# Kernel optimization log

Hardware: AMD Instinct MI355X
Metric: run time of the kernel (lower is better)

Reference implementation:

```python
import jax, jax.numpy as jnp
import numpy as np

B, S, D, H = 2, 2048, 1024, 16
HD = D // H  # head_dim = 64


def setup_inputs() -> dict:
    key = jax.random.key(0)
    ks = jax.random.split(key, 10)
    sc = 1.0 / np.sqrt(D)
    x = jax.random.normal(ks[0], (B, S, D), dtype=jnp.float32)
    # causal mask, 0 = masked (module does masked_fill(mask == 0, -1e9))
    mask = jnp.broadcast_to(jnp.tril(jnp.ones((S, S), dtype=jnp.int32)), (B, S, S))
    return {
        "x": x,
        "mask": mask,
        "Wq": jax.random.normal(ks[1], (D, D), dtype=jnp.float32) * sc,
        "bq": jnp.zeros((D,), dtype=jnp.float32),
        "Wk": jax.random.normal(ks[2], (D, D), dtype=jnp.float32) * sc,
        "bk": jnp.zeros((D,), dtype=jnp.float32),
        "Wv": jax.random.normal(ks[3], (D, D), dtype=jnp.float32) * sc,
        "bv": jnp.zeros((D,), dtype=jnp.float32),
        "Wo": jax.random.normal(ks[4], (D, D), dtype=jnp.float32) * sc,
        "bo": jnp.zeros((D,), dtype=jnp.float32),
    }


def reference(x, mask, Wq, bq, Wk, bk, Wv, bv, Wo, bo):
    b, s, _ = x.shape
    # torch nn.Linear: y = x @ W.T + b
    def split_heads(t):
        return t.reshape(b, s, H, HD).transpose(0, 2, 1, 3)  # [B,H,S,hd]
    q = split_heads(x @ Wq.T + bq)
    k = split_heads(x @ Wk.T + bk)
    v = split_heads(x @ Wv.T + bv)
    scores = jnp.einsum("bhqd,bhkd->bhqk", q, k) / jnp.sqrt(jnp.float32(HD))
    scores = jnp.where(mask[:, None, :, :] == 0, jnp.float32(-1e9), scores)
    w = jax.nn.softmax(scores, axis=-1)
    out = jnp.einsum("bhqk,bhkd->bhqd", w, v)  # [B,H,S,hd]
    out = out.transpose(0, 2, 1, 3).reshape(b, s, D)
    return out @ Wo.T + bo
```

## Files before the change

kernel.cpp:

```cpp
#include <hip/hip_runtime.h>
#include <cstdint>


typedef __bf16 bf16x8 __attribute__((ext_vector_type(8)));
typedef float f32x4 __attribute__((ext_vector_type(4)));

__device__ inline f32x4 mfma16(bf16x8 a, bf16x8 b, f32x4 c) {
    return __builtin_amdgcn_mfma_f32_16x16x32_bf16(a, b, c, 0, 0, 0);
}

__device__ inline uint16_t f2bf(float f) {
    uint32_t u = __builtin_bit_cast(uint32_t, f);
    u += 0x7FFFu + ((u >> 16) & 1u);
    return (uint16_t)(u >> 16);
}

__device__ inline void gload_lds16(const uint16_t* g, uint16_t* l) {
    __builtin_amdgcn_global_load_lds(
        (const __attribute__((address_space(1))) uint32_t*)g,
        (__attribute__((address_space(3))) uint32_t*)l, 16, 0, 0);
}

__global__ __launch_bounds__(256) void cast_all(const float* __restrict__ x,
                                                const float* __restrict__ wq,
                                                const float* __restrict__ wk,
                                                const float* __restrict__ wv,
                                                const float* __restrict__ wo,
                                                uint16_t* __restrict__ xbf,
                                                uint16_t* __restrict__ wbf) {
    int i = blockIdx.x * 256 + threadIdx.x;
    float4 v;
    uint64_t* dp;
    if (i < (1 << 20)) {
        v = ((const float4*)x)[i];
        dp = (uint64_t*)xbf + i;
    } else {
        int j = i - (1 << 20);
        const float* ws[4] = {wq, wk, wv, wo};
        v = ((const float4*)ws[j >> 18])[j & 0x3FFFF];
        dp = (uint64_t*)wbf + j;
    }
    uint64_t p = (uint64_t)f2bf(v.x) | ((uint64_t)f2bf(v.y) << 16) |
                 ((uint64_t)f2bf(v.z) << 32) | ((uint64_t)f2bf(v.w) << 48);
    *dp = p;
}

template<int OUTF32>
__global__ __launch_bounds__(256) void gemm128(const uint16_t* __restrict__ A,
                                               const uint16_t* __restrict__ W,
                                               const float* __restrict__ b0,
                                               const float* __restrict__ b1,
                                               const float* __restrict__ b2,
                                               void* __restrict__ o0,
                                               void* __restrict__ o1,
                                               void* __restrict__ o2,
                                               int K, float s0, float s1, float s2) {
    __shared__ __align__(16) uint16_t Alds[2][128 * 32];
    __shared__ __align__(16) uint16_t Blds[2][128 * 32];
    const int tid = threadIdx.x;
    const int lane = tid & 63, w = tid >> 6;
    const int l16 = lane & 15, quad = lane >> 4;
    const int wm = w & 1, wn = w >> 1;
    const int m0 = blockIdx.x * 128, n0 = blockIdx.y * 128;

    f32x4 acc[4][4] = {};

    const int ci0 = w * 128 + lane;
    const uint16_t* ga0 = A + (size_t)(m0 + (ci0 >> 2)) * K + (ci0 & 3) * 8;
    const uint16_t* gb0 = W + (size_t)(n0 + (ci0 >> 2)) * K + (ci0 & 3) * 8;
    const int ci1 = ci0 + 64;
    const uint16_t* ga1 = A + (size_t)(m0 + (ci1 >> 2)) * K + (ci1 & 3) * 8;
    const uint16_t* gb1 = W + (size_t)(n0 + (ci1 >> 2)) * K + (ci1 & 3) * 8;

    gload_lds16(ga0, Alds[0] + (w * 2 + 0) * 512);
    gload_lds16(gb0, Blds[0] + (w * 2 + 0) * 512);
    gload_lds16(ga1, Alds[0] + (w * 2 + 1) * 512);
    gload_lds16(gb1, Blds[0] + (w * 2 + 1) * 512);

    const int niter = K >> 5;
    for (int i = 0; i < niter; ++i) {
        __syncthreads();
        if (i + 1 < niter) {
            const int k1 = (i + 1) << 5;
            uint16_t* Ad = Alds[(i + 1) & 1];
            uint16_t* Bd = Blds[(i + 1) & 1];
            gload_lds16(ga0 + k1, Ad + (w * 2 + 0) * 512);
            gload_lds16(gb0 + k1, Bd + (w * 2 + 0) * 512);
            gload_lds16(ga1 + k1, Ad + (w * 2 + 1) * 512);
            gload_lds16(gb1 + k1, Bd + (w * 2 + 1) * 512);
        }
        const uint16_t* Ab = Alds[i & 1];
        const uint16_t* Bb = Blds[i & 1];
        bf16x8 af[4], bw[4];
#pragma unroll
        for (int t = 0; t < 4; ++t) {
            af[t] = *(const bf16x8*)(Ab + (wm * 64 + t * 16 + l16) * 32 + quad * 8);
            bw[t] = *(const bf16x8*)(Bb + (wn * 64 + t * 16 + l16) * 32 + quad * 8);
        }
#pragma unroll
        for (int mt = 0; mt < 4; ++mt)
#pragma unroll
            for (int nt = 0; nt < 4; ++nt)
                acc[mt][nt] = mfma16(af[mt], bw[nt], acc[mt][nt]);
    }

#pragma unroll
    for (int nt = 0; nt < 4; ++nt) {
        int col = n0 + wn * 64 + nt * 16 + l16;
        int seg = col >> 10, lcol = col & 1023;
        const float* bp = (seg == 0) ? b0 : (seg == 1 ? b1 : b2);
        float scale    = (seg == 0) ? s0 : (seg == 1 ? s1 : s2);
        void* op       = (seg == 0) ? o0 : (seg == 1 ? o1 : o2);
        float bc = bp[lcol];
#pragma unroll
        for (int mt = 0; mt < 4; ++mt)
#pragma unroll
            for (int r = 0; r < 4; ++r) {
                int row = m0 + wm * 64 + mt * 16 + quad * 4 + r;
                float v = (acc[mt][nt][r] + bc) * scale;
                if (OUTF32) ((float*)op)[(size_t)row * 1024 + lcol] = v;
                else        ((uint16_t*)op)[(size_t)row * 1024 + lcol] = f2bf(v);
            }
    }
}

__global__ __launch_bounds__(256) void transpose_v(const uint16_t* __restrict__ V,
                                                   uint16_t* __restrict__ Vt) {
    __shared__ __align__(16) uint16_t T[64 * 72];
    const int s0 = blockIdx.x * 64;
    const int bh = blockIdx.y;
    const int b = bh >> 4, h = bh & 15;
    const int tid = threadIdx.x;
    const int r = tid >> 2, c = tid & 3;
#pragma unroll
    for (int half = 0; half < 2; ++half) {
        uint4 v = *(const uint4*)(V + (size_t)(b * 2048 + s0 + r) * 1024 + h * 64 + half * 32 + c * 8);
        *(uint4*)(T + r * 72 + half * 32 + c * 8) = v;
    }
    __syncthreads();
#pragma unroll
    for (int it = 0; it < 2; ++it) {
        int id = it * 256 + tid;
        int d = id >> 3, c8 = (id & 7) * 8;
        uint32_t wpk[4];
#pragma unroll
        for (int jj = 0; jj < 4; ++jj) {
            uint32_t lo = T[(c8 + 2 * jj) * 72 + d];
            uint32_t hi = T[(c8 + 2 * jj + 1) * 72 + d];
            wpk[jj] = lo | (hi << 16);
        }
        uint4 o; o.x = wpk[0]; o.y = wpk[1]; o.z = wpk[2]; o.w = wpk[3];
        *(uint4*)(Vt + ((size_t)bh * 64 + d) * 2048 + s0 + c8) = o;
    }
}

__global__ __launch_bounds__(256) void attn_kernel(const uint16_t* __restrict__ Q,
                                                   const uint16_t* __restrict__ K,
                                                   const uint16_t* __restrict__ Vt,
                                                   uint16_t* __restrict__ att) {
    const int S = 2048, D = 1024;
    __shared__ __align__(16) uint16_t Klds[2][64 * 72];
    __shared__ __align__(16) uint16_t Vlds[2][64 * 72];
    __shared__ __align__(16) uint16_t Plds[4 * 32 * 72];

    const int bh = blockIdx.y;
    const int qb = (bh & 16) ? (int)blockIdx.x : 15 - (int)blockIdx.x;
    const int niter = 2 * qb + 2, kb_diag = 2 * qb;

    const int b = bh >> 4, h = bh & 15;
    const int tid = threadIdx.x, lane = tid & 63, w = tid >> 6;
    const int l16 = lane & 15, quad = lane >> 4;
    const int q0 = qb * 128;
    const size_t baseQK = (size_t)b * S * D + h * 64;
    uint16_t* Pw = Plds + w * (32 * 72);

    bf16x8 aq[2][2];
#pragma unroll
    for (int mt = 0; mt < 2; ++mt)
#pragma unroll
        for (int c = 0; c < 2; ++c)
            aq[mt][c] = *(const bf16x8*)(Q + baseQK +
                (size_t)(q0 + w * 32 + mt * 16 + l16) * D + c * 32 + quad * 8);

    bf16x8 ones;
#pragma unroll
    for (int j = 0; j < 8; ++j) ones[j] = (__bf16)1.0f;

    f32x4 accO[2][4] = {};
    f32x4 accL[2] = {};

    const int srow = tid >> 2, scq = tid & 3;
    const uint16_t* Kg = K + baseQK + (size_t)srow * D + scq * 16;
    const uint16_t* Vg = Vt + ((size_t)bh * 64 + srow) * S + scq * 16;
    const int soff = srow * 72 + scq * 16;

    uint4 kA, kB, vA, vB;
    kA = *(const uint4*)Kg; kB = *(const uint4*)(Kg + 8);
    vA = *(const uint4*)Vg; vB = *(const uint4*)(Vg + 8);
    *(uint4*)(Klds[0] + soff)     = kA;
    *(uint4*)(Klds[0] + soff + 8) = kB;
    *(uint4*)(Vlds[0] + soff)     = vA;
    *(uint4*)(Vlds[0] + soff + 8) = vB;
    {
        const uint16_t* kg = Kg + (size_t)64 * D;
        const uint16_t* vg = Vg + 64;
        kA = *(const uint4*)kg; kB = *(const uint4*)(kg + 8);
        vA = *(const uint4*)vg; vB = *(const uint4*)(vg + 8);
    }
    __syncthreads();

    for (int kb = 0; kb < niter; ++kb) {
        const uint16_t* Kb = Klds[kb & 1];
        const uint16_t* Vb = Vlds[kb & 1];

        if (kb + 1 < niter) {
            uint16_t* Kd = (uint16_t*)Klds[(kb + 1) & 1];
            uint16_t* Vd = (uint16_t*)Vlds[(kb + 1) & 1];
            *(uint4*)(Kd + soff)     = kA;
            *(uint4*)(Kd + soff + 8) = kB;
            *(uint4*)(Vd + soff)     = vA;
            *(uint4*)(Vd + soff + 8) = vB;
            if (kb + 2 < niter) {
                const uint16_t* kg = Kg + (size_t)((kb + 2) * 64) * D;
                const uint16_t* vg = Vg + (kb + 2) * 64;
                kA = *(const uint4*)kg; kB = *(const uint4*)(kg + 8);
                vA = *(const uint4*)vg; vB = *(const uint4*)(vg + 8);
            }
        }

        f32x4 sc[2][4];
#pragma unroll
        for (int t = 0; t < 4; ++t) {
            bf16x8 bk0 = *(const bf16x8*)(Kb + (t * 16 + l16) * 72 + quad * 8);
            bf16x8 bk1 = *(const bf16x8*)(Kb + (t * 16 + l16) * 72 + 32 + quad * 8);
            f32x4 z0 = {}; f32x4 z1 = {};
            sc[0][t] = mfma16(aq[0][1], bk1, mfma16(aq[0][0], bk0, z0));
            sc[1][t] = mfma16(aq[1][1], bk1, mfma16(aq[1][0], bk0, z1));
        }

        bf16x8 bv0[4], bv1[4];
#pragma unroll
        for (int nt = 0; nt < 4; ++nt) {
            bv0[nt] = *(const bf16x8*)(Vb + (nt * 16 + l16) * 72 + quad * 8);
            bv1[nt] = *(const bf16x8*)(Vb + (nt * 16 + l16) * 72 + 32 + quad * 8);
        }

        if (kb < kb_diag) {
#pragma unroll
            for (int mt = 0; mt < 2; ++mt)
#pragma unroll
                for (int r = 0; r < 4; ++r)
#pragma unroll
                    for (int t = 0; t < 4; ++t) {
                        float p = __builtin_amdgcn_exp2f(sc[mt][t][r]);
                        Pw[(mt * 16 + quad * 4 + r) * 72 + t * 16 + l16] =
                            (uint16_t)(__builtin_bit_cast(uint32_t, p) >> 16);
                    }
        } else {
#pragma unroll
            for (int mt = 0; mt < 2; ++mt)
#pragma unroll
                for (int r = 0; r < 4; ++r) {
                    const int qrow = q0 + w * 32 + mt * 16 + quad * 4 + r;
#pragma unroll
                    for (int t = 0; t < 4; ++t) {
                        float s = sc[mt][t][r];
                        int kcol = kb * 64 + t * 16 + l16;
                        if (kcol > qrow) s = -1e30f;
                        float p = __builtin_amdgcn_exp2f(s);
                        Pw[(mt * 16 + quad * 4 + r) * 72 + t * 16 + l16] =
                            (uint16_t)(__builtin_bit_cast(uint32_t, p) >> 16);
                    }
                }
        }

        __asm__ volatile("s_waitcnt lgkmcnt(0)" ::: "memory");

        bf16x8 ap0[2], ap1[2];
#pragma unroll
        for (int mt = 0; mt < 2; ++mt) {
            ap0[mt] = *(const bf16x8*)(Pw + (mt * 16 + l16) * 72 + quad * 8);
            ap1[mt] = *(const bf16x8*)(Pw + (mt * 16 + l16) * 72 + 32 + quad * 8);
        }
#pragma unroll
        for (int nt = 0; nt < 4; ++nt) {
            accO[0][nt] = mfma16(ap1[0], bv1[nt], mfma16(ap0[0], bv0[nt], accO[0][nt]));
            accO[1][nt] = mfma16(ap1[1], bv1[nt], mfma16(ap0[1], bv0[nt], accO[1][nt]));
        }
        accL[0] = mfma16(ap1[0], ones, mfma16(ap0[0], ones, accL[0]));
        accL[1] = mfma16(ap1[1], ones, mfma16(ap0[1], ones, accL[1]));

        if (kb + 1 < niter) __syncthreads();
    }

#pragma unroll
    for (int mt = 0; mt < 2; ++mt)
#pragma unroll
        for (int r = 0; r < 4; ++r) {
            const int qrow = q0 + w * 32 + mt * 16 + quad * 4 + r;
            float inv = __builtin_amdgcn_rcpf(accL[mt][r]);
            uint16_t* ob = att + (size_t)(b * S + qrow) * 1024 + h * 64 + l16;
#pragma unroll
            for (int nt = 0; nt < 4; ++nt)
                ob[nt * 16] = f2bf(accO[mt][nt][r] * inv);
        }
}

extern "C" void kernel_launch(void* const* d_in, const int* in_sizes, int n_in,
                              void* d_out, int out_size, void* d_ws, size_t ws_size,
                              hipStream_t stream) {
    const float* x  = (const float*)d_in[0];
    const float* Wq = (const float*)d_in[2];
    const float* bq = (const float*)d_in[3];
    const float* Wk = (const float*)d_in[4];
    const float* bk = (const float*)d_in[5];
    const float* Wv = (const float*)d_in[6];
    const float* bv = (const float*)d_in[7];
    const float* Wo = (const float*)d_in[8];
    const float* bo = (const float*)d_in[9];
    float* out = (float*)d_out;

    const int B = 2, S = 2048, D = 1024, H = 16;
    const int M = B * S;

    uint8_t* w = (uint8_t*)d_ws;
    uint16_t* xbf  = (uint16_t*)(w);
    uint16_t* wqbf = (uint16_t*)(w + (size_t)( 8 << 20));
    uint16_t* qbf  = (uint16_t*)(w + (size_t)(16 << 20));
    uint16_t* kbf  = (uint16_t*)(w + (size_t)(24 << 20));
    uint16_t* vbf  = (uint16_t*)(w + (size_t)(32 << 20));
    uint16_t* vtbf = (uint16_t*)(w + (size_t)(40 << 20));
    uint16_t* wobf = wqbf + (size_t)3 * D * D;
    uint16_t* attbf = xbf;

    cast_all<<<dim3((1 << 21) / 256), dim3(256), 0, stream>>>(
        x, Wq, Wk, Wv, Wo, xbf, wqbf);

    gemm128<0><<<dim3(M / 128, 3072 / 128), dim3(256), 0, stream>>>(
        xbf, wqbf, bq, bk, bv, qbf, kbf, vbf, D, 0.125f * 1.44269504f, 1.0f, 1.0f);

    transpose_v<<<dim3(S / 64, B * H), dim3(256), 0, stream>>>(vbf, vtbf);

    attn_kernel<<<dim3(16, B * H), dim3(256), 0, stream>>>(qbf, kbf, vtbf, attbf);

    gemm128<1><<<dim3(M / 128, 1024 / 128), dim3(256), 0, stream>>>(
        attbf, wobf, bo, bo, bo, out, out, out, D, 1.0f, 1.0f, 1.0f);
}
```

Measured before the change: 206.1 us.

## Stage GEMM and attention epilogues through LDS; use narrower N tile for output GEMM

The bf16 QKV GEMM epilogue now writes results into shared memory and then stores full 16-byte rows to global memory, replacing scattered 2-byte stores. The attention kernel does the same through its per-wave P buffer before writing the output rows. The output projection GEMM is templated to a 64-wide N tile, which doubles the number of blocks to improve occupancy across CUs. The trade-offs are extra LDS round trips and barriers, plus lower per-block reuse in the output GEMM.

```diff
diff --git a/kernel.cpp b/kernel.cpp
--- a/kernel.cpp
+++ b/kernel.cpp
@@ -45,7 +45,7 @@
     *dp = p;
 }
 
-template<int OUTF32>
+template<int OUTF32, int BN>
 __global__ __launch_bounds__(256) void gemm128(const uint16_t* __restrict__ A,
                                                const uint16_t* __restrict__ W,
                                                const float* __restrict__ b0,
@@ -55,72 +55,110 @@
                                                void* __restrict__ o1,
                                                void* __restrict__ o2,
                                                int K, float s0, float s1, float s2) {
-    __shared__ __align__(16) uint16_t Alds[2][128 * 32];
-    __shared__ __align__(16) uint16_t Blds[2][128 * 32];
+    constexpr int NT = BN / 32;
+    __shared__ __align__(16) uint16_t SH[2][(128 + BN) * 32];
     const int tid = threadIdx.x;
     const int lane = tid & 63, w = tid >> 6;
     const int l16 = lane & 15, quad = lane >> 4;
     const int wm = w & 1, wn = w >> 1;
-    const int m0 = blockIdx.x * 128, n0 = blockIdx.y * 128;
-
-    f32x4 acc[4][4] = {};
+    const int m0 = blockIdx.x * 128, n0 = blockIdx.y * BN;
+
+    f32x4 acc[4][NT] = {};
 
     const int ci0 = w * 128 + lane;
     const uint16_t* ga0 = A + (size_t)(m0 + (ci0 >> 2)) * K + (ci0 & 3) * 8;
-    const uint16_t* gb0 = W + (size_t)(n0 + (ci0 >> 2)) * K + (ci0 & 3) * 8;
     const int ci1 = ci0 + 64;
     const uint16_t* ga1 = A + (size_t)(m0 + (ci1 >> 2)) * K + (ci1 & 3) * 8;
+    const uint16_t* gb0 = W + (size_t)(n0 + (ci0 >> 2)) * K + (ci0 & 3) * 8;
     const uint16_t* gb1 = W + (size_t)(n0 + (ci1 >> 2)) * K + (ci1 & 3) * 8;
-
-    gload_lds16(ga0, Alds[0] + (w * 2 + 0) * 512);
-    gload_lds16(gb0, Blds[0] + (w * 2 + 0) * 512);
-    gload_lds16(ga1, Alds[0] + (w * 2 + 1) * 512);
-    gload_lds16(gb1, Blds[0] + (w * 2 + 1) * 512);
+    const uint16_t* gbS = W + (size_t)(n0 + (tid >> 2)) * K + (tid & 3) * 8;
+
+    uint16_t* A0 = SH[0];
+    uint16_t* B0 = SH[0] + 128 * 32;
+    uint16_t* A1 = SH[1];
+    uint16_t* B1 = SH[1] + 128 * 32;
+
+    gload_lds16(ga0, A0 + (w * 2 + 0) * 512);
+    gload_lds16(ga1, A0 + (w * 2 + 1) * 512);
+    if constexpr (BN == 128) {
+        gload_lds16(gb0, B0 + (w * 2 + 0) * 512);
+        gload_lds16(gb1, B0 + (w * 2 + 1) * 512);
+    } else {
+        gload_lds16(gbS, B0 + w * 512);
+    }
 
     const int niter = K >> 5;
     for (int i = 0; i < niter; ++i) {
         __syncthreads();
         if (i + 1 < niter) {
             const int k1 = (i + 1) << 5;
-            uint16_t* Ad = Alds[(i + 1) & 1];
-            uint16_t* Bd = Blds[(i + 1) & 1];
+            uint16_t* Ad = (i & 1) ? A0 : A1;
+            uint16_t* Bd = (i & 1) ? B0 : B1;
             gload_lds16(ga0 + k1, Ad + (w * 2 + 0) * 512);
-            gload_lds16(gb0 + k1, Bd + (w * 2 + 0) * 512);
             gload_lds16(ga1 + k1, Ad + (w * 2 + 1) * 512);
-            gload_lds16(gb1 + k1, Bd + (w * 2 + 1) * 512);
-        }
-        const uint16_t* Ab = Alds[i & 1];
-        const uint16_t* Bb = Blds[i & 1];
-        bf16x8 af[4], bw[4];
-#pragma unroll
-        for (int t = 0; t < 4; ++t) {
+            if constexpr (BN == 128) {
+                gload_lds16(gb0 + k1, Bd + (w * 2 + 0) * 512);
+                gload_lds16(gb1 + k1, Bd + (w * 2 + 1) * 512);
+            } else {
+                gload_lds16(gbS + k1, Bd + w * 512);
+            }
+        }
+        const uint16_t* Ab = (i & 1) ? A1 : A0;
+        const uint16_t* Bb = (i & 1) ? B1 : B0;
+        bf16x8 af[4], bw[NT];
+#pragma unroll
+        for (int t = 0; t < 4; ++t)
             af[t] = *(const bf16x8*)(Ab + (wm * 64 + t * 16 + l16) * 32 + quad * 8);
-            bw[t] = *(const bf16x8*)(Bb + (wn * 64 + t * 16 + l16) * 32 + quad * 8);
-        }
+#pragma unroll
+        for (int t = 0; t < NT; ++t)
+            bw[t] = *(const bf16x8*)(Bb + (wn * (BN / 2) + t * 16 + l16) * 32 + quad * 8);
 #pragma unroll
         for (int mt = 0; mt < 4; ++mt)
 #pragma unroll
-            for (int nt = 0; nt < 4; ++nt)
+            for (int nt = 0; nt < NT; ++nt)
                 acc[mt][nt] = mfma16(af[mt], bw[nt], acc[mt][nt]);
     }
 
-#pragma unroll
-    for (int nt = 0; nt < 4; ++nt) {
-        int col = n0 + wn * 64 + nt * 16 + l16;
-        int seg = col >> 10, lcol = col & 1023;
-        const float* bp = (seg == 0) ? b0 : (seg == 1 ? b1 : b2);
-        float scale    = (seg == 0) ? s0 : (seg == 1 ? s1 : s2);
-        void* op       = (seg == 0) ? o0 : (seg == 1 ? o1 : o2);
-        float bc = bp[lcol];
-#pragma unroll
-        for (int mt = 0; mt < 4; ++mt)
-#pragma unroll
-            for (int r = 0; r < 4; ++r) {
-                int row = m0 + wm * 64 + mt * 16 + quad * 4 + r;
-                float v = (acc[mt][nt][r] + bc) * scale;
-                if (OUTF32) ((float*)op)[(size_t)row * 1024 + lcol] = v;
-                else        ((uint16_t*)op)[(size_t)row * 1024 + lcol] = f2bf(v);
-            }
+    const int seg = n0 >> 10, lc0 = n0 & 1023;
+    const float* bp = (seg == 0) ? b0 : (seg == 1 ? b1 : b2);
+    const float scale = (seg == 0) ? s0 : (seg == 1 ? s1 : s2);
+    void* op = (seg == 0) ? o0 : (seg == 1 ? o1 : o2);
+
+    if constexpr (OUTF32) {
+#pragma unroll
+        for (int nt = 0; nt < NT; ++nt) {
+            int lcol = lc0 + wn * (BN / 2) + nt * 16 + l16;
+            float bc = bp[lcol];
+#pragma unroll
+            for (int mt = 0; mt < 4; ++mt)
+#pragma unroll
+                for (int r = 0; r < 4; ++r) {
+                    int row = m0 + wm * 64 + mt * 16 + quad * 4 + r;
+                    ((float*)op)[(size_t)row * 1024 + lcol] = (acc[mt][nt][r] + bc) * scale;
+                }
+        }
+    } else {
+        __syncthreads();
+        uint16_t* EP = &SH[0][0];
+#pragma unroll
+        for (int nt = 0; nt < NT; ++nt) {
+            float bc = bp[lc0 + wn * (BN / 2) + nt * 16 + l16];
+#pragma unroll
+            for (int mt = 0; mt < 4; ++mt)
+#pragma unroll
+                for (int r = 0; r < 4; ++r)
+                    EP[(wm * 64 + mt * 16 + quad * 4 + r) * 128 +
+                       wn * (BN / 2) + nt * 16 + l16] =
+                        f2bf((acc[mt][nt][r] + bc) * scale);
+        }
+        __syncthreads();
+#pragma unroll
+        for (int p = 0; p < 8; ++p) {
+            int row = p * 16 + (tid >> 4);
+            int c8 = (tid & 15) * 8;
+            uint4 v = *(const uint4*)(EP + row * 128 + c8);
+            *(uint4*)((uint16_t*)op + (size_t)(m0 + row) * 1024 + lc0 + c8) = v;
+        }
     }
 }
 
@@ -293,17 +331,25 @@
         if (kb + 1 < niter) __syncthreads();
     }
 
+    __asm__ volatile("s_waitcnt lgkmcnt(0)" ::: "memory");
 #pragma unroll
     for (int mt = 0; mt < 2; ++mt)
 #pragma unroll
         for (int r = 0; r < 4; ++r) {
-            const int qrow = q0 + w * 32 + mt * 16 + quad * 4 + r;
             float inv = __builtin_amdgcn_rcpf(accL[mt][r]);
-            uint16_t* ob = att + (size_t)(b * S + qrow) * 1024 + h * 64 + l16;
+            const int rl = mt * 16 + quad * 4 + r;
 #pragma unroll
             for (int nt = 0; nt < 4; ++nt)
-                ob[nt * 16] = f2bf(accO[mt][nt][r] * inv);
-        }
+                Pw[rl * 72 + nt * 16 + l16] = f2bf(accO[mt][nt][r] * inv);
+        }
+    __asm__ volatile("s_waitcnt lgkmcnt(0)" ::: "memory");
+#pragma unroll
+    for (int p = 0; p < 4; ++p) {
+        int row = p * 8 + (lane >> 3);
+        int c8 = (lane & 7) * 8;
+        uint4 v = *(const uint4*)(Pw + row * 72 + c8);
+        *(uint4*)(att + (size_t)(b * S + q0 + w * 32 + row) * 1024 + h * 64 + c8) = v;
+    }
 }
 
 extern "C" void kernel_launch(void* const* d_in, const int* in_sizes, int n_in,
@@ -336,13 +382,13 @@
     cast_all<<<dim3((1 << 21) / 256), dim3(256), 0, stream>>>(
         x, Wq, Wk, Wv, Wo, xbf, wqbf);
 
-    gemm128<0><<<dim3(M / 128, 3072 / 128), dim3(256), 0, stream>>>(
+    gemm128<0, 128><<<dim3(M / 128, 3072 / 128), dim3(256), 0, stream>>>(
         xbf, wqbf, bq, bk, bv, qbf, kbf, vbf, D, 0.125f * 1.44269504f, 1.0f, 1.0f);
 
     transpose_v<<<dim3(S / 64, B * H), dim3(256), 0, stream>>>(vbf, vtbf);
 
     attn_kernel<<<dim3(16, B * H), dim3(256), 0, stream>>>(qbf, kbf, vtbf, attbf);
 
-    gemm128<1><<<dim3(M / 128, 1024 / 128), dim3(256), 0, stream>>>(
+    gemm128<1, 64><<<dim3(M / 128, 1024 / 64), dim3(256), 0, stream>>>(
         attbf, wobf, bo, bo, bo, out, out, out, D, 1.0f, 1.0f, 1.0f);
 }
```

New measurement: 197.9 us. 4.0% less time.
